# Kernel tuning notes

Measured on AMD Instinct MI355X. Metric: run time of the kernel, lower is better.

The kernel has to match this reference:

```python
import jax, jax.numpy as jnp
import numpy as np

N, IN_DIM, OUT_DIM = 8192, 256, 64
NEG_BIG = -9e15
LRELU_SLOPE = 0.01  # torch F.leaky_relu default


def setup_inputs() -> dict:
    key = jax.random.key(0)
    k1, k2, k3, k4 = jax.random.split(key, 4)
    inp = jax.random.normal(k1, (N, IN_DIM), dtype=jnp.float32)
    adj = jax.random.randint(k2, (N, N), 0, 2, dtype=jnp.int32)
    # xavier_uniform with gain=1.414
    limW = 1.414 * np.sqrt(6.0 / (IN_DIM + OUT_DIM))
    W = jax.random.uniform(k3, (IN_DIM, OUT_DIM), minval=-limW, maxval=limW, dtype=jnp.float32)
    lima = 1.414 * np.sqrt(6.0 / (2 * OUT_DIM + 1))
    a = jax.random.uniform(k4, (2 * OUT_DIM, 1), minval=-lima, maxval=lima, dtype=jnp.float32)
    return {"input": inp, "adj": adj, "W": W, "a": a}


def reference(input, adj, W, a):
    h = input @ W                      # [N, D]
    a1, a2 = a[:OUT_DIM, 0], a[OUT_DIM:, 0]
    # e[i,j] = leaky_relu(a1.h_i + a2.h_j) == the concat-based score, no NxNx2D tensor
    f1 = h @ a1                        # [N]
    f2 = h @ a2                        # [N]
    e = jax.nn.leaky_relu(f1[:, None] + f2[None, :], negative_slope=LRELU_SLOPE)  # [N, N]
    face_Rhand = e[1, 2]
    face_Lhand = e[1, 3]
    Rhand_Lhand = e[3, 2]
    attention = jnp.where(adj > 0, e, jnp.float32(NEG_BIG))
    alpha = jax.nn.softmax(attention, axis=1)
    h_prime = alpha @ h                # [N, D]
    return (h_prime, face_Rhand, face_Lhand, Rhand_Lhand)
```

## Files before the change

### kernel.cpp

```cpp
#include <hip/hip_runtime.h>
#include <hip/hip_bf16.h>

#define GN 8192
#define KD 256
#define OD 64
#define LOG2E 1.44269504f
#define NCH 16

typedef __attribute__((ext_vector_type(8))) short bf16x8;
typedef __attribute__((ext_vector_type(4))) float f32x4;

__device__ __forceinline__ float fexp2(float x) {
#if __has_builtin(__builtin_amdgcn_exp2f)
  return __builtin_amdgcn_exp2f(x);
#else
  return exp2f(x);
#endif
}

__global__ __launch_bounds__(256) void gat_k1(
    const float* __restrict__ input, const float* __restrict__ W,
    const float* __restrict__ a, __hip_bfloat16* __restrict__ hTt,
    float* __restrict__ f1p, float* __restrict__ f2p, float* __restrict__ out)
{
  __shared__ float Wl[KD * OD];
  __shared__ float inT[KD * 33];
  __shared__ float red1[8][32];
  __shared__ float red2[8][32];
  __shared__ float s1row[32];
  __shared__ float s2row[32];

  const int tid = threadIdx.x;
  const int i0 = blockIdx.x * 32;

  for (int idx = tid; idx < KD * OD / 4; idx += 256)
    ((float4*)Wl)[idx] = ((const float4*)W)[idx];

#pragma unroll
  for (int it = 0; it < 8; ++it) {
    int idx = tid + it * 256;
    int r = idx >> 6, k4 = idx & 63;
    float4 v = *(const float4*)(input + (long)(i0 + r) * KD + k4 * 4);
    inT[(k4 * 4 + 0) * 33 + r] = v.x;
    inT[(k4 * 4 + 1) * 33 + r] = v.y;
    inT[(k4 * 4 + 2) * 33 + r] = v.z;
    inT[(k4 * 4 + 3) * 33 + r] = v.w;
  }
  __syncthreads();

  const int r = tid & 31;
  const int cg = tid >> 5;
  float acc[8];
#pragma unroll
  for (int c = 0; c < 8; ++c) acc[c] = 0.f;

#pragma unroll 4
  for (int k = 0; k < KD; ++k) {
    float inv = inT[k * 33 + r];
    float4 wa = *(const float4*)&Wl[k * 64 + cg * 8];
    float4 wb = *(const float4*)&Wl[k * 64 + cg * 8 + 4];
    acc[0] += inv * wa.x; acc[1] += inv * wa.y;
    acc[2] += inv * wa.z; acc[3] += inv * wa.w;
    acc[4] += inv * wb.x; acc[5] += inv * wb.y;
    acc[6] += inv * wb.z; acc[7] += inv * wb.w;
  }

#pragma unroll
  for (int c = 0; c < 8; ++c)
    hTt[(long)blockIdx.x * (OD * 32) + (cg * 8 + c) * 32 + r] =
        __float2bfloat16(acc[c]);

  float s1 = 0.f, s2 = 0.f;
#pragma unroll
  for (int c = 0; c < 8; ++c) {
    s1 += acc[c] * a[cg * 8 + c];
    s2 += acc[c] * a[OD + cg * 8 + c];
  }
  red1[cg][r] = s1; red2[cg][r] = s2;
  __syncthreads();
  if (tid < 32) {
    float f1 = 0.f, f2 = 0.f;
#pragma unroll
    for (int g = 0; g < 8; ++g) { f1 += red1[g][tid]; f2 += red2[g][tid]; }
    s1row[tid] = f1; s2row[tid] = f2;
    f1p[i0 + tid] = f1 * LOG2E;
    f2p[i0 + tid] = f2 * LOG2E;
  }
  __syncthreads();
  if (blockIdx.x == 0 && tid == 0) {
    float e12 = s1row[1] + s2row[2];
    float e13 = s1row[1] + s2row[3];
    float e32 = s1row[3] + s2row[2];
    out[(long)GN * OD + 0] = fmaxf(e12, 0.01f * e12);
    out[(long)GN * OD + 1] = fmaxf(e13, 0.01f * e13);
    out[(long)GN * OD + 2] = fmaxf(e32, 0.01f * e32);
  }
}

__global__ __launch_bounds__(256, 4) void gat_k2(
    const int* __restrict__ adj, const __hip_bfloat16* __restrict__ hTt,
    const float* __restrict__ f1p, const float* __restrict__ f2p,
    float* __restrict__ pn, float* __restrict__ pd)
{
  __shared__ float f2l[4096];
  __shared__ float pb[4 * 16 * 68];
  __shared__ float sb[64];

  const int tid = threadIdx.x;
  const int lane = tid & 63;
  const int wv = tid >> 6;
  const int tn = lane & 15;
  const int quad = lane >> 4;
  const int rg = blockIdx.x >> 1;
  const int js = blockIdx.x & 1;
  const int i0 = rg * 16;
  const int jbase = js * 4096;

  for (int i = tid; i < 4096 / 4; i += 256)
    ((float4*)f2l)[i] = ((const float4*)(f2p + jbase))[i];

  const float f1r = f1p[i0 + tn];

  const int jo0 = wv * 64 + quad * 8;
  const int jo1 = jo0 + 32;
  const int* __restrict__ adjr = adj + (long)(i0 + tn) * GN + jbase;
  const __hip_bfloat16* hsl = hTt + (long)(jbase / 32) * (OD * 32) + tn * 32 + quad * 8;

  f32x4 acc[4];
#pragma unroll
  for (int nf = 0; nf < 4; ++nf) acc[nf] = (f32x4){0.f, 0.f, 0.f, 0.f};
  f32x4 accS = (f32x4){0.f, 0.f, 0.f, 0.f};

  bf16x8 ones;
  {
    short ov = (tn == 0) ? (short)0x3F80 : (short)0;
#pragma unroll
    for (int i = 0; i < 8; ++i) ones[i] = ov;
  }

  __syncthreads();

  for (int c = 0; c < NCH; ++c) {
    const int* ap = adjr + c * 256;
    const int4 a0 = *(const int4*)(ap + jo0);
    const int4 a1 = *(const int4*)(ap + jo0 + 4);
    const int4 a2 = *(const int4*)(ap + jo1);
    const int4 a3 = *(const int4*)(ap + jo1 + 4);

    const __hip_bfloat16* h0 = hsl + (long)(c * 8 + 2 * wv) * (OD * 32);
    const __hip_bfloat16* h1 = h0 + (OD * 32);
    bf16x8 B0[4], B1[4];
#pragma unroll
    for (int nf = 0; nf < 4; ++nf) {
      B0[nf] = *(const bf16x8*)(h0 + nf * (16 * 32));
      B1[nf] = *(const bf16x8*)(h1 + nf * (16 * 32));
    }

    const float4 f20 = *(const float4*)&f2l[c * 256 + jo0];
    const float4 f21 = *(const float4*)&f2l[c * 256 + jo0 + 4];
    const float4 f22 = *(const float4*)&f2l[c * 256 + jo1];
    const float4 f23 = *(const float4*)&f2l[c * 256 + jo1 + 4];

    union { bf16x8 v; unsigned u[4]; } w0, w1;
    {
      float e0 = f1r + f20.x, e1 = f1r + f20.y, e2 = f1r + f20.z, e3 = f1r + f20.w;
      float e4 = f1r + f21.x, e5 = f1r + f21.y, e6 = f1r + f21.z, e7 = f1r + f21.w;
      float v0 = fexp2((a0.x > 0) ? fmaxf(e0, 0.01f * e0) : -256.f);
      float v1 = fexp2((a0.y > 0) ? fmaxf(e1, 0.01f * e1) : -256.f);
      float v2 = fexp2((a0.z > 0) ? fmaxf(e2, 0.01f * e2) : -256.f);
      float v3 = fexp2((a0.w > 0) ? fmaxf(e3, 0.01f * e3) : -256.f);
      float v4 = fexp2((a1.x > 0) ? fmaxf(e4, 0.01f * e4) : -256.f);
      float v5 = fexp2((a1.y > 0) ? fmaxf(e5, 0.01f * e5) : -256.f);
      float v6 = fexp2((a1.z > 0) ? fmaxf(e6, 0.01f * e6) : -256.f);
      float v7 = fexp2((a1.w > 0) ? fmaxf(e7, 0.01f * e7) : -256.f);
      w0.u[0] = __builtin_amdgcn_perm(__float_as_uint(v1), __float_as_uint(v0), 0x07060302u);
      w0.u[1] = __builtin_amdgcn_perm(__float_as_uint(v3), __float_as_uint(v2), 0x07060302u);
      w0.u[2] = __builtin_amdgcn_perm(__float_as_uint(v5), __float_as_uint(v4), 0x07060302u);
      w0.u[3] = __builtin_amdgcn_perm(__float_as_uint(v7), __float_as_uint(v6), 0x07060302u);
    }
    {
      float e0 = f1r + f22.x, e1 = f1r + f22.y, e2 = f1r + f22.z, e3 = f1r + f22.w;
      float e4 = f1r + f23.x, e5 = f1r + f23.y, e6 = f1r + f23.z, e7 = f1r + f23.w;
      float v0 = fexp2((a2.x > 0) ? fmaxf(e0, 0.01f * e0) : -256.f);
      float v1 = fexp2((a2.y > 0) ? fmaxf(e1, 0.01f * e1) : -256.f);
      float v2 = fexp2((a2.z > 0) ? fmaxf(e2, 0.01f * e2) : -256.f);
      float v3 = fexp2((a2.w > 0) ? fmaxf(e3, 0.01f * e3) : -256.f);
      float v4 = fexp2((a3.x > 0) ? fmaxf(e4, 0.01f * e4) : -256.f);
      float v5 = fexp2((a3.y > 0) ? fmaxf(e5, 0.01f * e5) : -256.f);
      float v6 = fexp2((a3.z > 0) ? fmaxf(e6, 0.01f * e6) : -256.f);
      float v7 = fexp2((a3.w > 0) ? fmaxf(e7, 0.01f * e7) : -256.f);
      w1.u[0] = __builtin_amdgcn_perm(__float_as_uint(v1), __float_as_uint(v0), 0x07060302u);
      w1.u[1] = __builtin_amdgcn_perm(__float_as_uint(v3), __float_as_uint(v2), 0x07060302u);
      w1.u[2] = __builtin_amdgcn_perm(__float_as_uint(v5), __float_as_uint(v4), 0x07060302u);
      w1.u[3] = __builtin_amdgcn_perm(__float_as_uint(v7), __float_as_uint(v6), 0x07060302u);
    }

#pragma unroll
    for (int nf = 0; nf < 4; ++nf)
      acc[nf] = __builtin_amdgcn_mfma_f32_16x16x32_bf16(w0.v, B0[nf], acc[nf], 0, 0, 0);
    accS = __builtin_amdgcn_mfma_f32_16x16x32_bf16(w0.v, ones, accS, 0, 0, 0);
#pragma unroll
    for (int nf = 0; nf < 4; ++nf)
      acc[nf] = __builtin_amdgcn_mfma_f32_16x16x32_bf16(w1.v, B1[nf], acc[nf], 0, 0, 0);
    accS = __builtin_amdgcn_mfma_f32_16x16x32_bf16(w1.v, ones, accS, 0, 0, 0);
  }

#pragma unroll
  for (int nf = 0; nf < 4; ++nf)
#pragma unroll
    for (int rgi = 0; rgi < 4; ++rgi)
      pb[(wv * 16 + quad * 4 + rgi) * 68 + nf * 16 + tn] = acc[nf][rgi];
  if (tn == 0) {
#pragma unroll
    for (int rgi = 0; rgi < 4; ++rgi)
      sb[wv * 16 + quad * 4 + rgi] = accS[rgi];
  }
  __syncthreads();
  for (int t = tid; t < 16 * OD; t += 256) {
    int rr = t >> 6, cc = t & 63;
    float num = pb[(0 * 16 + rr) * 68 + cc] + pb[(1 * 16 + rr) * 68 + cc] +
                pb[(2 * 16 + rr) * 68 + cc] + pb[(3 * 16 + rr) * 68 + cc];
    pn[((long)js * GN + i0 + rr) * OD + cc] = num;
  }
  if (tid < 16) {
    float den = sb[0 * 16 + tid] + sb[1 * 16 + tid] + sb[2 * 16 + tid] + sb[3 * 16 + tid];
    pd[(long)js * GN + i0 + tid] = den;
  }
}

__global__ __launch_bounds__(256) void gat_k3(
    const float* __restrict__ pn, const float* __restrict__ pd,
    float* __restrict__ out)
{
  long t = (long)blockIdx.x * 256 + threadIdx.x;
  int i = (int)(t >> 6);
  float num = pn[t] + pn[(long)GN * OD + t];
  float den = pd[i] + pd[GN + i];
  out[t] = num / den;
}

extern "C" void kernel_launch(void* const* d_in, const int* in_sizes, int n_in,
                              void* d_out, int out_size, void* d_ws, size_t ws_size,
                              hipStream_t stream) {
  const float* input = (const float*)d_in[0];
  const int* adj     = (const int*)d_in[1];
  const float* W     = (const float*)d_in[2];
  const float* a     = (const float*)d_in[3];
  float* out = (float*)d_out;

  char* ws = (char*)d_ws;
  __hip_bfloat16* hTt = (__hip_bfloat16*)ws;
  float* f1p = (float*)(ws + (size_t)OD * GN * 2);
  float* f2p = f1p + GN;
  float* pn  = f2p + GN;
  float* pd  = pn + (size_t)2 * GN * OD;

  gat_k1<<<256, 256, 0, stream>>>(input, W, a, hTt, f1p, f2p, out);
  gat_k2<<<1024, 256, 0, stream>>>(adj, hTt, f1p, f2p, pn, pd);
  gat_k3<<<GN * OD / 256, 256, 0, stream>>>(pn, pd, out);
}
```

Measured before the change: 393.1 us.

## Drop split-K partials, fuse normalization into attention kernel, restructure projection kernel

The attention kernel now has each block cover the full 8192-column row range instead of half, so it normalizes numerator by denominator itself and writes the output directly. This removes the third kernel and the partial-sum round trip through workspace. The projection kernel is rewritten to do 64 rows per block, read W from global memory and stage the transposed bf16 h tile through shared memory for coalesced stores. The cost is half as many attention blocks (512), longer per-block loops, a larger f2 LDS buffer and a lower occupancy hint, which may reduce latency hiding on the adjacency stream.

Result: slower. 429.6 us (+9.3%).

```diff
diff --git a/kernel.cpp b/kernel.cpp
--- a/kernel.cpp
+++ b/kernel.cpp
@@ -5,7 +5,7 @@
 #define KD 256
 #define OD 64
 #define LOG2E 1.44269504f
-#define NCH 16
+#define NCH2 32
 
 typedef __attribute__((ext_vector_type(8))) short bf16x8;
 typedef __attribute__((ext_vector_type(4))) float f32x4;
@@ -23,70 +23,84 @@
     const float* __restrict__ a, __hip_bfloat16* __restrict__ hTt,
     float* __restrict__ f1p, float* __restrict__ f2p, float* __restrict__ out)
 {
-  __shared__ float Wl[KD * OD];
-  __shared__ float inT[KD * 33];
-  __shared__ float red1[8][32];
-  __shared__ float red2[8][32];
-  __shared__ float s1row[32];
-  __shared__ float s2row[32];
+  __shared__ float inT[64 * 261];
+  __shared__ float red1[4][64];
+  __shared__ float red2[4][64];
+  __shared__ float s1row[64];
+  __shared__ float s2row[64];
 
   const int tid = threadIdx.x;
-  const int i0 = blockIdx.x * 32;
-
-  for (int idx = tid; idx < KD * OD / 4; idx += 256)
-    ((float4*)Wl)[idx] = ((const float4*)W)[idx];
-
-#pragma unroll
-  for (int it = 0; it < 8; ++it) {
+  const int lane = tid & 63;
+  const int wv = __builtin_amdgcn_readfirstlane(tid >> 6);
+  const int i0 = blockIdx.x * 64;
+
+#pragma unroll
+  for (int it = 0; it < 16; ++it) {
     int idx = tid + it * 256;
     int r = idx >> 6, k4 = idx & 63;
     float4 v = *(const float4*)(input + (long)(i0 + r) * KD + k4 * 4);
-    inT[(k4 * 4 + 0) * 33 + r] = v.x;
-    inT[(k4 * 4 + 1) * 33 + r] = v.y;
-    inT[(k4 * 4 + 2) * 33 + r] = v.z;
-    inT[(k4 * 4 + 3) * 33 + r] = v.w;
-  }
-  __syncthreads();
-
-  const int r = tid & 31;
-  const int cg = tid >> 5;
-  float acc[8];
-#pragma unroll
-  for (int c = 0; c < 8; ++c) acc[c] = 0.f;
-
-#pragma unroll 4
+    float* d = &inT[r * 261 + k4 * 4];
+    d[0] = v.x; d[1] = v.y; d[2] = v.z; d[3] = v.w;
+  }
+  __syncthreads();
+
+  const float* __restrict__ Wp = W + wv * 16;
+  const float* inrow = &inT[lane * 261];
+  float acc[16];
+#pragma unroll
+  for (int i = 0; i < 16; ++i) acc[i] = 0.f;
+
+#pragma unroll 2
   for (int k = 0; k < KD; ++k) {
-    float inv = inT[k * 33 + r];
-    float4 wa = *(const float4*)&Wl[k * 64 + cg * 8];
-    float4 wb = *(const float4*)&Wl[k * 64 + cg * 8 + 4];
-    acc[0] += inv * wa.x; acc[1] += inv * wa.y;
-    acc[2] += inv * wa.z; acc[3] += inv * wa.w;
-    acc[4] += inv * wb.x; acc[5] += inv * wb.y;
-    acc[6] += inv * wb.z; acc[7] += inv * wb.w;
-  }
-
-#pragma unroll
-  for (int c = 0; c < 8; ++c)
-    hTt[(long)blockIdx.x * (OD * 32) + (cg * 8 + c) * 32 + r] =
-        __float2bfloat16(acc[c]);
+    float inv = inrow[k];
+    float4 w0 = *(const float4*)(Wp + k * 64 + 0);
+    float4 w1 = *(const float4*)(Wp + k * 64 + 4);
+    float4 w2 = *(const float4*)(Wp + k * 64 + 8);
+    float4 w3 = *(const float4*)(Wp + k * 64 + 12);
+    acc[0]  += inv * w0.x; acc[1]  += inv * w0.y;
+    acc[2]  += inv * w0.z; acc[3]  += inv * w0.w;
+    acc[4]  += inv * w1.x; acc[5]  += inv * w1.y;
+    acc[6]  += inv * w1.z; acc[7]  += inv * w1.w;
+    acc[8]  += inv * w2.x; acc[9]  += inv * w2.y;
+    acc[10] += inv * w2.z; acc[11] += inv * w2.w;
+    acc[12] += inv * w3.x; acc[13] += inv * w3.y;
+    acc[14] += inv * w3.z; acc[15] += inv * w3.w;
+  }
 
   float s1 = 0.f, s2 = 0.f;
 #pragma unroll
-  for (int c = 0; c < 8; ++c) {
-    s1 += acc[c] * a[cg * 8 + c];
-    s2 += acc[c] * a[OD + cg * 8 + c];
-  }
-  red1[cg][r] = s1; red2[cg][r] = s2;
-  __syncthreads();
-  if (tid < 32) {
-    float f1 = 0.f, f2 = 0.f;
-#pragma unroll
-    for (int g = 0; g < 8; ++g) { f1 += red1[g][tid]; f2 += red2[g][tid]; }
+  for (int i = 0; i < 16; ++i) {
+    s1 += acc[i] * a[wv * 16 + i];
+    s2 += acc[i] * a[OD + wv * 16 + i];
+  }
+  red1[wv][lane] = s1; red2[wv][lane] = s2;
+  __syncthreads();
+
+  if (tid < 64) {
+    float f1 = red1[0][tid] + red1[1][tid] + red1[2][tid] + red1[3][tid];
+    float f2 = red2[0][tid] + red2[1][tid] + red2[2][tid] + red2[3][tid];
     s1row[tid] = f1; s2row[tid] = f2;
     f1p[i0 + tid] = f1 * LOG2E;
     f2p[i0 + tid] = f2 * LOG2E;
   }
-  __syncthreads();
+
+  __hip_bfloat16* sT = (__hip_bfloat16*)inT;
+#pragma unroll
+  for (int i = 0; i < 16; ++i)
+    sT[(wv * 16 + i) * 72 + lane] = __float2bfloat16(acc[i]);
+  __syncthreads();
+
+  {
+    int jt = tid >> 7;
+    int col = (tid >> 1) & 63;
+    int jm0 = (tid & 1) * 16;
+    const int4* sp =
+        (const int4*)((const unsigned short*)inT + col * 72 + jt * 32 + jm0);
+    int4 p0 = sp[0], p1 = sp[1];
+    int4* dst = (int4*)(hTt + (long)blockIdx.x * 4096 + jt * 2048 + col * 32 + jm0);
+    dst[0] = p0; dst[1] = p1;
+  }
+
   if (blockIdx.x == 0 && tid == 0) {
     float e12 = s1row[1] + s2row[2];
     float e13 = s1row[1] + s2row[3];
@@ -97,12 +111,12 @@
   }
 }
 
-__global__ __launch_bounds__(256, 4) void gat_k2(
+__global__ __launch_bounds__(256, 2) void gat_k2(
     const int* __restrict__ adj, const __hip_bfloat16* __restrict__ hTt,
     const float* __restrict__ f1p, const float* __restrict__ f2p,
-    float* __restrict__ pn, float* __restrict__ pd)
+    float* __restrict__ out)
 {
-  __shared__ float f2l[4096];
+  __shared__ float f2l[8192];
   __shared__ float pb[4 * 16 * 68];
   __shared__ float sb[64];
 
@@ -111,20 +125,17 @@
   const int wv = tid >> 6;
   const int tn = lane & 15;
   const int quad = lane >> 4;
-  const int rg = blockIdx.x >> 1;
-  const int js = blockIdx.x & 1;
-  const int i0 = rg * 16;
-  const int jbase = js * 4096;
-
-  for (int i = tid; i < 4096 / 4; i += 256)
-    ((float4*)f2l)[i] = ((const float4*)(f2p + jbase))[i];
+  const int i0 = blockIdx.x * 16;
+
+  for (int i = tid; i < 8192 / 4; i += 256)
+    ((float4*)f2l)[i] = ((const float4*)f2p)[i];
 
   const float f1r = f1p[i0 + tn];
 
   const int jo0 = wv * 64 + quad * 8;
   const int jo1 = jo0 + 32;
-  const int* __restrict__ adjr = adj + (long)(i0 + tn) * GN + jbase;
-  const __hip_bfloat16* hsl = hTt + (long)(jbase / 32) * (OD * 32) + tn * 32 + quad * 8;
+  const int* __restrict__ adjr = adj + (long)(i0 + tn) * GN;
+  const __hip_bfloat16* hsl = hTt + tn * 32 + quad * 8;
 
   f32x4 acc[4];
 #pragma unroll
@@ -140,7 +151,7 @@
 
   __syncthreads();
 
-  for (int c = 0; c < NCH; ++c) {
+  for (int c = 0; c < NCH2; ++c) {
     const int* ap = adjr + c * 256;
     const int4 a0 = *(const int4*)(ap + jo0);
     const int4 a1 = *(const int4*)(ap + jo0 + 4);
@@ -220,23 +231,9 @@
     int rr = t >> 6, cc = t & 63;
     float num = pb[(0 * 16 + rr) * 68 + cc] + pb[(1 * 16 + rr) * 68 + cc] +
                 pb[(2 * 16 + rr) * 68 + cc] + pb[(3 * 16 + rr) * 68 + cc];
-    pn[((long)js * GN + i0 + rr) * OD + cc] = num;
-  }
-  if (tid < 16) {
-    float den = sb[0 * 16 + tid] + sb[1 * 16 + tid] + sb[2 * 16 + tid] + sb[3 * 16 + tid];
-    pd[(long)js * GN + i0 + tid] = den;
-  }
-}
-
-__global__ __launch_bounds__(256) void gat_k3(
-    const float* __restrict__ pn, const float* __restrict__ pd,
-    float* __restrict__ out)
-{
-  long t = (long)blockIdx.x * 256 + threadIdx.x;
-  int i = (int)(t >> 6);
-  float num = pn[t] + pn[(long)GN * OD + t];
-  float den = pd[i] + pd[GN + i];
-  out[t] = num / den;
+    float den = sb[0 * 16 + rr] + sb[1 * 16 + rr] + sb[2 * 16 + rr] + sb[3 * 16 + rr];
+    out[((long)(i0 + rr)) * OD + cc] = num / den;
+  }
 }
 
 extern "C" void kernel_launch(void* const* d_in, const int* in_sizes, int n_in,
@@ -252,10 +249,7 @@
   __hip_bfloat16* hTt = (__hip_bfloat16*)ws;
   float* f1p = (float*)(ws + (size_t)OD * GN * 2);
   float* f2p = f1p + GN;
-  float* pn  = f2p + GN;
-  float* pd  = pn + (size_t)2 * GN * OD;
-
-  gat_k1<<<256, 256, 0, stream>>>(input, W, a, hTt, f1p, f2p, out);
-  gat_k2<<<1024, 256, 0, stream>>>(adj, hTt, f1p, f2p, pn, pd);
-  gat_k3<<<GN * OD / 256, 256, 0, stream>>>(pn, pd, out);
-}
+
+  gat_k1<<<128, 256, 0, stream>>>(input, W, a, hTt, f1p, f2p, out);
+  gat_k2<<<512, 256, 0, stream>>>(adj, hTt, f1p, f2p, out);
+}
```
